# Kernel tuning notes

Measured on AMD Instinct MI355X. Metric: run time of the kernel, lower is better.

## Reference

```python
import jax, jax.numpy as jnp
import numpy as np


def setup_inputs() -> dict:
    key = jax.random.key(0)
    k1, k2, k3, k4 = jax.random.split(key, 4)
    N, E, C_in, C_out = 100000, 1600000, 256, 128
    x = jax.random.normal(k1, (N, C_in), dtype=jnp.float32)
    edge_index = jax.random.randint(k2, (2, E), 0, N, dtype=jnp.int64)
    W = jax.random.normal(k3, (C_in, C_out), dtype=jnp.float32) * 0.05
    b = jax.random.normal(k4, (C_out,), dtype=jnp.float32) * 0.05
    return {"x": x, "edge_index": edge_index, "W": W, "b": b}


def reference(x, edge_index, W, b):
    # GCNConv (PyG defaults): add self-loops, symmetric normalization,
    # linear transform, scatter-sum aggregation, bias; then ReLU (norm=None).
    N = x.shape[0]
    loops = jnp.arange(N, dtype=edge_index.dtype)
    src = jnp.concatenate([edge_index[0], loops])  # [E+N] message sources (x_j)
    dst = jnp.concatenate([edge_index[1], loops])  # [E+N] aggregation targets

    deg = jax.ops.segment_sum(jnp.ones_like(dst, dtype=x.dtype), dst, num_segments=N)
    deg_inv_sqrt = jnp.where(deg > 0, jax.lax.rsqrt(jnp.maximum(deg, 1.0)), 0.0)
    norm = deg_inv_sqrt[src] * deg_inv_sqrt[dst]  # [E+N]

    h = x @ W                                      # [N, C_out]
    msg = h[src] * norm[:, None]                   # [E+N, C_out] gather + scale
    out = jax.ops.segment_sum(msg, dst, num_segments=N) + b  # scatter-add
    return jax.nn.relu(out)
```

## Files before the change

### kernel.cpp

```cpp
#include <hip/hip_runtime.h>


typedef __attribute__((ext_vector_type(8))) short bf16x8;
typedef __attribute__((ext_vector_type(4))) float f32x4;

__device__ __forceinline__ unsigned short f2bf(float f) {
  unsigned int u = __float_as_uint(f);
  u += 0x7FFFu + ((u >> 16) & 1u);
  return (unsigned short)(u >> 16);
}
__device__ __forceinline__ float bfval(unsigned short h) {
  return __uint_as_float(((unsigned int)h) << 16);
}
__device__ __forceinline__ float bf0(unsigned int u) { return __uint_as_float(u << 16); }
__device__ __forceinline__ float bf1(unsigned int u) { return __uint_as_float(u & 0xFFFF0000u); }

__global__ __launch_bounds__(256) void k_wprep(
    const float* __restrict__ W, unsigned short* __restrict__ blob)
{
  int g = blockIdx.x * 256 + threadIdx.x;
  if (g >= 256 * 128) return;
  int k = g >> 7, c = g & 127;
  float w = W[g];
  unsigned short hi = f2bf(w);
  unsigned short lo = f2bf(w - bfval(hi));
  int q = k >> 5, kk = k & 31;
  unsigned lin = (unsigned)(c * 64 + kk * 2);
  unsigned swz = lin ^ (((unsigned)(c & 7)) << 4);
  blob[(q * 16384 + swz) >> 1] = hi;
  blob[(q * 16384 + 8192 + swz) >> 1] = lo;
}

__global__ __launch_bounds__(256) void k_gemm_scatter(
    const float* __restrict__ x, const unsigned char* __restrict__ wblob,
    unsigned short* __restrict__ h, int N,
    const int* __restrict__ src, const int* __restrict__ dst,
    unsigned int* __restrict__ cnt, int* __restrict__ srcs, int E,
    int gemmB, int scatB)
{
  __shared__ __align__(16) unsigned char smem[20480];

  const int id = blockIdx.x;
  bool isGemm;
  int idx;
  if (scatB == 2 * gemmB) {
    if (id % 3 == 0) { isGemm = true;  idx = id / 3; }
    else             { isGemm = false; idx = id - 1 - id / 3; }
  } else {
    isGemm = id < gemmB;
    idx = isGemm ? id : id - gemmB;
  }

  const int tid = threadIdx.x;

  if (!isGemm) {
    if (idx < scatB) {
      int e = idx * 256 + tid;
      if (e < E) {
        int d = dst[e];
        int pos = (int)atomicAdd(&cnt[d], 1u);
        if (pos < 64) srcs[((size_t)d << 6) + pos] = src[e];
      }
    }
    return;
  }
  if (idx >= gemmB) return;

  const int row0 = idx * 32;
  const int lane = tid & 63;
  const int wv = tid >> 6;
  const int mb = wv & 1;
  const int nb = wv >> 1;

  f32x4 acc[4] = {};

  const int ar = tid >> 3;
  const int akk0 = (tid & 7) * 4;
  int arow = row0 + ar; if (arow >= N) arow = N - 1;
  const unsigned aaddr = ((unsigned)(ar * 64 + akk0 * 2)) ^ (((unsigned)(ar & 7)) << 4);

  const int rr = 16 * mb + (lane & 15);
  const unsigned aoff = ((unsigned)(rr * 64 + (lane >> 4) * 16)) ^ (((unsigned)(rr & 7)) << 4);

  for (int q = 0; q < 8; ++q) {
    {
      const float4 v = *(const float4*)(x + (size_t)arow * 256 + q * 32 + akk0);
      unsigned short h0 = f2bf(v.x), h1 = f2bf(v.y), h2 = f2bf(v.z), h3 = f2bf(v.w);
      unsigned short l0 = f2bf(v.x - bfval(h0));
      unsigned short l1 = f2bf(v.y - bfval(h1));
      unsigned short l2 = f2bf(v.z - bfval(h2));
      unsigned short l3 = f2bf(v.w - bfval(h3));
      *(uint2*)(smem + 16384 + aaddr) =
          make_uint2((unsigned)h0 | ((unsigned)h1 << 16), (unsigned)h2 | ((unsigned)h3 << 16));
      *(uint2*)(smem + 18432 + aaddr) =
          make_uint2((unsigned)l0 | ((unsigned)l1 << 16), (unsigned)l2 | ((unsigned)l3 << 16));
    }
    {
      const uint4* gb = (const uint4*)(wblob + (size_t)q * 16384);
      uint4* sb = (uint4*)smem;
      uint4 t0 = gb[tid], t1 = gb[tid + 256], t2 = gb[tid + 512], t3 = gb[tid + 768];
      sb[tid] = t0; sb[tid + 256] = t1; sb[tid + 512] = t2; sb[tid + 768] = t3;
    }
    __syncthreads();
    {
      const bf16x8 ah = *(const bf16x8*)(smem + 16384 + aoff);
      const bf16x8 al = *(const bf16x8*)(smem + 18432 + aoff);
      #pragma unroll
      for (int nf = 0; nf < 4; ++nf) {
        const int c = 64 * nb + 16 * nf + (lane & 15);
        const unsigned boff =
            ((unsigned)(c * 64 + (lane >> 4) * 16)) ^ (((unsigned)(c & 7)) << 4);
        const bf16x8 bh = *(const bf16x8*)(smem + boff);
        const bf16x8 bl = *(const bf16x8*)(smem + 8192 + boff);
        acc[nf] = __builtin_amdgcn_mfma_f32_16x16x32_bf16(ah, bh, acc[nf], 0, 0, 0);
        acc[nf] = __builtin_amdgcn_mfma_f32_16x16x32_bf16(ah, bl, acc[nf], 0, 0, 0);
        acc[nf] = __builtin_amdgcn_mfma_f32_16x16x32_bf16(al, bh, acc[nf], 0, 0, 0);
      }
    }
    __syncthreads();
  }

  #pragma unroll
  for (int nf = 0; nf < 4; ++nf) {
    const int col = 64 * nb + 16 * nf + (lane & 15);
    #pragma unroll
    for (int r = 0; r < 4; ++r) {
      const int row = row0 + 16 * mb + 4 * (lane >> 4) + r;
      if (row < N) h[(size_t)row * 128 + col] = f2bf(acc[nf][r]);
    }
  }
}

__global__ __launch_bounds__(256) void k_aggr(
    const unsigned short* __restrict__ h, const int* __restrict__ srcs,
    const unsigned int* __restrict__ cnt,
    const float* __restrict__ b, float* __restrict__ out, int N)
{
  const int wid = (int)(((size_t)blockIdx.x * 256 + threadIdx.x) >> 6);
  if (wid >= N) return;
  const int lane = threadIdx.x & 63;
  const int eg = lane >> 4;
  const int cl = lane & 15;
  const int deg = min((int)cnt[wid], 64);
  const int m = deg + 1;
  const size_t coff = (size_t)(cl << 3);
  const size_t lbase = (size_t)wid << 6;

  float a0 = 0.f, a1 = 0.f, a2 = 0.f, a3 = 0.f, a4 = 0.f, a5 = 0.f, a6 = 0.f, a7 = 0.f;

  for (int base = 0; base < m; base += 64) {
    const int kk = min(64, m - base);
    const int slot = base + lane;
    int sidx = wid;
    if (slot < deg) sidx = srcs[lbase + slot];
    const float sd = rsqrtf((float)(cnt[sidx] + 1u));
    int j = 0;
    for (; j + 8 <= kk; j += 8) {
      const int s0 = __shfl(sidx, j + eg, 64);
      const int s1 = __shfl(sidx, j + 4 + eg, 64);
      const float d0 = __shfl(sd, j + eg, 64);
      const float d1 = __shfl(sd, j + 4 + eg, 64);
      const uint4 v0 = *(const uint4*)(h + ((size_t)s0 << 7) + coff);
      const uint4 v1 = *(const uint4*)(h + ((size_t)s1 << 7) + coff);
      a0 = fmaf(bf0(v0.x), d0, a0); a1 = fmaf(bf1(v0.x), d0, a1);
      a2 = fmaf(bf0(v0.y), d0, a2); a3 = fmaf(bf1(v0.y), d0, a3);
      a4 = fmaf(bf0(v0.z), d0, a4); a5 = fmaf(bf1(v0.z), d0, a5);
      a6 = fmaf(bf0(v0.w), d0, a6); a7 = fmaf(bf1(v0.w), d0, a7);
      a0 = fmaf(bf0(v1.x), d1, a0); a1 = fmaf(bf1(v1.x), d1, a1);
      a2 = fmaf(bf0(v1.y), d1, a2); a3 = fmaf(bf1(v1.y), d1, a3);
      a4 = fmaf(bf0(v1.z), d1, a4); a5 = fmaf(bf1(v1.z), d1, a5);
      a6 = fmaf(bf0(v1.w), d1, a6); a7 = fmaf(bf1(v1.w), d1, a7);
    }
    for (; j < kk; j += 4) {
      const int s0 = __shfl(sidx, j + eg, 64);
      const float d0 = __shfl(sd, j + eg, 64);
      if (j + eg < kk) {
        const uint4 v0 = *(const uint4*)(h + ((size_t)s0 << 7) + coff);
        a0 = fmaf(bf0(v0.x), d0, a0); a1 = fmaf(bf1(v0.x), d0, a1);
        a2 = fmaf(bf0(v0.y), d0, a2); a3 = fmaf(bf1(v0.y), d0, a3);
        a4 = fmaf(bf0(v0.z), d0, a4); a5 = fmaf(bf1(v0.z), d0, a5);
        a6 = fmaf(bf0(v0.w), d0, a6); a7 = fmaf(bf1(v0.w), d0, a7);
      }
    }
  }

  a0 += __shfl_xor(a0, 16, 64); a0 += __shfl_xor(a0, 32, 64);
  a1 += __shfl_xor(a1, 16, 64); a1 += __shfl_xor(a1, 32, 64);
  a2 += __shfl_xor(a2, 16, 64); a2 += __shfl_xor(a2, 32, 64);
  a3 += __shfl_xor(a3, 16, 64); a3 += __shfl_xor(a3, 32, 64);
  a4 += __shfl_xor(a4, 16, 64); a4 += __shfl_xor(a4, 32, 64);
  a5 += __shfl_xor(a5, 16, 64); a5 += __shfl_xor(a5, 32, 64);
  a6 += __shfl_xor(a6, 16, 64); a6 += __shfl_xor(a6, 32, 64);
  a7 += __shfl_xor(a7, 16, 64); a7 += __shfl_xor(a7, 32, 64);

  if (lane < 32) {
    const float dn = rsqrtf((float)m);
    const int hi = lane >> 4;
    const int c0 = ((lane & 15) << 3) + (hi << 2);
    const float4 bb = *(const float4*)(b + c0);
    const float r0 = hi ? a4 : a0;
    const float r1 = hi ? a5 : a1;
    const float r2 = hi ? a6 : a2;
    const float r3 = hi ? a7 : a3;
    float4 o;
    o.x = fmaxf(fmaf(dn, r0, bb.x), 0.f);
    o.y = fmaxf(fmaf(dn, r1, bb.y), 0.f);
    o.z = fmaxf(fmaf(dn, r2, bb.z), 0.f);
    o.w = fmaxf(fmaf(dn, r3, bb.w), 0.f);
    *(float4*)(out + ((size_t)wid << 7) + c0) = o;
  }
}

extern "C" void kernel_launch(void* const* d_in, const int* in_sizes, int n_in,
                              void* d_out, int out_size, void* d_ws, size_t ws_size,
                              hipStream_t stream)
{
  const float* x  = (const float*)d_in[0];
  const int* ei   = (const int*)d_in[1];
  const float* W  = (const float*)d_in[2];
  const float* b  = (const float*)d_in[3];
  float* out = (float*)d_out;

  const int Cout = in_sizes[3];
  const int Cin  = in_sizes[2] / Cout;
  const int N    = in_sizes[0] / Cin;
  const int E    = in_sizes[1] / 2;

  const int* src = ei;
  const int* dst = ei + E;

  char* p = (char*)d_ws;
  size_t off = 0;
  auto alloc = [&](size_t bytes) { char* q = p + off; off = (off + bytes + 255) & ~(size_t)255; return q; };
  unsigned int* cnt = (unsigned int*)alloc((size_t)N * 4);
  int* srcs         = (int*)alloc((size_t)N * 64 * 4);
  unsigned short* h = (unsigned short*)alloc((size_t)N * Cout * 2);
  unsigned short* wblob = (unsigned short*)alloc(8 * 16384);

  const int gemmB = (N + 31) / 32;
  const int scatB = (E + 255) / 256;

  k_wprep<<<128, 256, 0, stream>>>(W, wblob);
  hipMemsetAsync(cnt, 0, (size_t)N * 4, stream);
  k_gemm_scatter<<<gemmB + scatB, 256, 0, stream>>>(x, (const unsigned char*)wblob, h, N,
                                                    src, dst, cnt, srcs, E,
                                                    gemmB, scatB);
  k_aggr<<<(N + 3) / 4, 256, 0, stream>>>(h, srcs, cnt, b, out, N);
}
```

Baseline: 327.4 us.

## Fold count reset into weight prep and batch edges per scatter block

The hipMemsetAsync of the per-node counters is removed and the zeroing is done inside the weight-prep kernel, which now launches enough threads to cover N. Each scatter block now handles 8 edges per thread, loading all indices before issuing the atomics, which gives more loads in flight and far fewer blocks. The interleaved GEMM/scatter block ordering is replaced by putting all scatter blocks first and the GEMM blocks after them. This cuts one launch and the per-block overhead, but changes how scatter and GEMM work overlap on the device.

```diff
diff --git a/kernel.cpp b/kernel.cpp
--- a/kernel.cpp
+++ b/kernel.cpp
@@ -16,9 +16,11 @@
 __device__ __forceinline__ float bf1(unsigned int u) { return __uint_as_float(u & 0xFFFF0000u); }
 
 __global__ __launch_bounds__(256) void k_wprep(
-    const float* __restrict__ W, unsigned short* __restrict__ blob)
+    const float* __restrict__ W, unsigned short* __restrict__ blob,
+    unsigned int* __restrict__ cnt, int N)
 {
   int g = blockIdx.x * 256 + threadIdx.x;
+  if (g < N) cnt[g] = 0u;
   if (g >= 256 * 128) return;
   int k = g >> 7, c = g & 127;
   float w = W[g];
@@ -41,29 +43,30 @@
   __shared__ __align__(16) unsigned char smem[20480];
 
   const int id = blockIdx.x;
-  bool isGemm;
-  int idx;
-  if (scatB == 2 * gemmB) {
-    if (id % 3 == 0) { isGemm = true;  idx = id / 3; }
-    else             { isGemm = false; idx = id - 1 - id / 3; }
-  } else {
-    isGemm = id < gemmB;
-    idx = isGemm ? id : id - gemmB;
-  }
-
+  const bool isGemm = id >= scatB;
   const int tid = threadIdx.x;
 
   if (!isGemm) {
-    if (idx < scatB) {
-      int e = idx * 256 + tid;
-      if (e < E) {
-        int d = dst[e];
-        int pos = (int)atomicAdd(&cnt[d], 1u);
-        if (pos < 64) srcs[((size_t)d << 6) + pos] = src[e];
+    const int e0 = id * 2048 + tid;
+    int d[8], s[8];
+    #pragma unroll
+    for (int i = 0; i < 8; ++i) {
+      const int e = e0 + i * 256;
+      const bool ok = e < E;
+      d[i] = ok ? dst[e] : -1;
+      s[i] = ok ? src[e] : 0;
+    }
+    #pragma unroll
+    for (int i = 0; i < 8; ++i) {
+      if (d[i] >= 0) {
+        int pos = (int)atomicAdd(&cnt[d[i]], 1u);
+        if (pos < 64) srcs[((size_t)d[i] << 6) + pos] = s[i];
       }
     }
     return;
   }
+
+  const int idx = id - scatB;
   if (idx >= gemmB) return;
 
   const int row0 = idx * 32;
@@ -238,11 +241,11 @@
   unsigned short* wblob = (unsigned short*)alloc(8 * 16384);
 
   const int gemmB = (N + 31) / 32;
-  const int scatB = (E + 255) / 256;
-
-  k_wprep<<<128, 256, 0, stream>>>(W, wblob);
-  hipMemsetAsync(cnt, 0, (size_t)N * 4, stream);
-  k_gemm_scatter<<<gemmB + scatB, 256, 0, stream>>>(x, (const unsigned char*)wblob, h, N,
+  const int scatB = (E + 2047) / 2048;
+
+  const int prepThreads = (N > 256 * 128) ? N : 256 * 128;
+  k_wprep<<<(prepThreads + 255) / 256, 256, 0, stream>>>(W, wblob, cnt, N);
+  k_gemm_scatter<<<scatB + gemmB, 256, 0, stream>>>(x, (const unsigned char*)wblob, h, N,
                                                     src, dst, cnt, srcs, E,
                                                     gemmB, scatB);
   k_aggr<<<(N + 3) / 4, 256, 0, stream>>>(h, srcs, cnt, b, out, N);
```

Result: slower. 421.0 us (+28.6%).
